# Performance work log

Hardware: AMD Instinct MI355X
Metric: run time of the kernel (lower is better)

## Reference

```python
import jax, jax.numpy as jnp
import numpy as np

# dims
C = 16      # input_channels
H = 64      # hidden_channels
HID = 128   # CDEFunc hidden width (hardcoded in source)
OUT = 1     # output_channels
L = 128     # number of time knots -> L-1 spline segments
B = 2048    # batch


def setup_inputs() -> dict:
    key = jax.random.key(0)
    ks = jax.random.split(key, 9)
    n = lambda k, shape, s: (jax.random.normal(k, shape, dtype=jnp.float32) * s)
    return {
        # cubic Hermite spline coeffs: concat(a, b, two_c, three_d) along last dim
        "coeffs": n(ks[0], (B, L - 1, 4 * C), 0.1),
        "W_init": n(ks[1], (H, C), 0.2),
        "b_init": jnp.zeros((H,), jnp.float32),
        "W1": n(ks[2], (HID, H), 0.1),
        "b1": jnp.zeros((HID,), jnp.float32),
        "W2": n(ks[3], (H * C, HID), 0.05),
        "b2": jnp.zeros((H * C,), jnp.float32),
        "W_out": n(ks[4], (OUT, H), 0.1),
        "b_out": jnp.zeros((OUT,), jnp.float32),
    }


def _spline_deriv(coeffs, t):
    """dX/dt of cubic spline at scalar time t. coeffs: (B, L-1, 4C)."""
    idx = jnp.clip(jnp.floor(t).astype(jnp.int32), 0, L - 2)
    seg = jax.lax.dynamic_slice_in_dim(coeffs, idx, 1, axis=1)[:, 0]  # (B, 4C)
    a, b, two_c, three_d = jnp.split(seg, 4, axis=-1)
    fr = t - idx.astype(t.dtype) if hasattr(t, 'dtype') else t - idx
    return b + two_c * fr + three_d * (fr * fr)  # (B, C)


def reference(coeffs, W_init, b_init, W1, b1, W2, b2, W_out, b_out):
    # X(0) = a of first segment (frac = 0)
    X0 = coeffs[:, 0, :C]
    z0 = X0 @ W_init.T + b_init  # (B, H)

    def f(z, dX):
        # CDEFunc: linear-relu-linear-tanh -> (B, H, C), then contract with dX/dt
        h = jax.nn.relu(z @ W1.T + b1)
        g = jnp.tanh(h @ W2.T + b2).reshape(-1, H, C)
        return jnp.einsum('bhc,bc->bh', g, dX)

    dt = jnp.float32(1.0)  # one RK4 step per knot interval

    def step(z, t):
        d0 = _spline_deriv(coeffs, t)
        dm = _spline_deriv(coeffs, t + 0.5 * dt)
        d1 = _spline_deriv(coeffs, t + dt)
        k1 = f(z, d0)
        k2 = f(z + 0.5 * dt * k1, dm)
        k3 = f(z + 0.5 * dt * k2, dm)
        k4 = f(z + dt * k3, d1)
        return z + (dt / 6.0) * (k1 + 2.0 * k2 + 2.0 * k3 + k4), None

    ts = jnp.arange(L - 1, dtype=jnp.float32)
    zT, _ = jax.lax.scan(step, z0, ts)
    return zT @ W_out.T + b_out  # (B, OUT)
```

## Files before the change

kernel.cpp:

```cpp
#include <hip/hip_runtime.h>

#define L_DIM 128
#define BB 8

typedef _Float16 f16;
typedef _Float16 f16x8 __attribute__((ext_vector_type(8)));
typedef float f32x4 __attribute__((ext_vector_type(4)));

__device__ __forceinline__ float fast_tanh_b(float x, float bk) {
    float e = __builtin_amdgcn_exp2f(fmaf(x, 2.8853900817779268f, bk));
    float r = __builtin_amdgcn_rcpf(e + 1.0f);
    return fmaf(-2.0f, r, 1.0f);
}

__attribute__((amdgpu_flat_work_group_size(512, 512), amdgpu_waves_per_eu(2)))
__global__ void
cde_kernel(const float* __restrict__ coeffs,
           const float* __restrict__ W_init, const float* __restrict__ b_init,
           const float* __restrict__ W1, const float* __restrict__ b1,
           const float* __restrict__ W2, const float* __restrict__ b2,
           const float* __restrict__ W_out, const float* __restrict__ b_out,
           float* __restrict__ out)
{
    __shared__ __align__(16) f16   z16[16][72];
    __shared__ __align__(16) f16   h16[16][136];
    __shared__ __align__(16) float dxT[2][3][16][20];
    __shared__ __align__(16) float zf[BB][64];

    const int tid  = threadIdx.x;
    const int blk  = blockIdx.x;
    const int lane = tid & 63;
    const int w    = tid >> 6;
    const int q    = lane >> 4;
    const int lr   = lane & 15;
    const int hh   = w * 8 + (lr & 7);
    const int chp  = lr >> 3;
    const int row0 = (q & 1) * 4 + (q >> 1) * 2;

    f16x8 w2f[8][4];
    float b2k[8];
#pragma unroll
    for (int t8 = 0; t8 < 8; ++t8) {
        const int outc = hh * 16 + 2 * t8 + chp;
        b2k[t8] = 2.8853900817779268f * b2[outc];
#pragma unroll
        for (int kc = 0; kc < 4; ++kc) {
            const float* src = W2 + (size_t)outc * 128 + kc * 32 + q * 8;
            f16x8 v;
#pragma unroll
            for (int i = 0; i < 8; ++i) v[i] = (f16)src[i];
            w2f[t8][kc] = v;
        }
    }
    f16x8 w1f[2];
#pragma unroll
    for (int kc = 0; kc < 2; ++kc) {
        const float* src = W1 + (size_t)(w * 16 + lr) * 64 + kc * 32 + q * 8;
        f16x8 v;
#pragma unroll
        for (int i = 0; i < 8; ++i) v[i] = (f16)src[i];
        w1f[kc] = v;
    }
    const float b1r = b1[w * 16 + lr];

    float z32r[2], ksumr[2];
#pragma unroll
    for (int j = 0; j < 2; ++j) {
        const float* x0 = coeffs + (size_t)(blk * BB + row0 + j) * (L_DIM - 1) * 64;
        float a = b_init[hh];
#pragma unroll
        for (int c = 0; c < 16; ++c) a = fmaf(x0[c], W_init[hh * 16 + c], a);
        z32r[j] = a;
        ksumr[j] = 0.f;
        if (lr < 8) z16[row0 + j][hh] = (f16)a;
    }
    for (int i = tid; i < 8 * 72; i += 512) z16[8 + i / 72][i % 72] = (f16)0.f;
    if (tid < BB * 16) {
        const int b = tid >> 4, c = tid & 15;
        const float* seg = coeffs + (size_t)(blk * BB + b) * (L_DIM - 1) * 64;
        float bv = seg[16 + c], cv = seg[32 + c], dv = seg[48 + c];
        dxT[0][0][c][b] = bv;
        dxT[0][1][c][b] = fmaf(0.25f, dv, fmaf(0.5f, cv, bv));
        dxT[0][2][c][b] = seg[64 + 16 + c];
    }
    __syncthreads();

    for (int t = 0; t < L_DIM - 1; ++t) {
        const int buf = t & 1;
        float pb = 0.f, pc = 0.f, pd = 0.f, pe = 0.f;
#pragma unroll 1
        for (int s = 0; s < 4; ++s) {
            {
                f16x8 za0 = *(const f16x8*)&z16[lr][q * 8];
                f16x8 za1 = *(const f16x8*)&z16[lr][32 + q * 8];
                f32x4 hacc = {0.f, 0.f, 0.f, 0.f};
                hacc = __builtin_amdgcn_mfma_f32_16x16x32_f16(za0, w1f[0], hacc, 0, 0, 0);
                hacc = __builtin_amdgcn_mfma_f32_16x16x32_f16(za1, w1f[1], hacc, 0, 0, 0);
#pragma unroll
                for (int r = 0; r < 4; ++r)
                    h16[q * 4 + r][w * 16 + lr] = (f16)fmaxf(hacc[r] + b1r, 0.f);
            }
            __syncthreads();

            const int ds = (s + 1) >> 1;
            const f16x8 af0 = *(const f16x8*)&h16[lr][q * 8];
            const f16x8 af1 = *(const f16x8*)&h16[lr][32 + q * 8];
            const f16x8 af2 = *(const f16x8*)&h16[lr][64 + q * 8];
            const f16x8 af3 = *(const f16x8*)&h16[lr][96 + q * 8];
            f32x4 acc[8];
#pragma unroll
            for (int t8 = 0; t8 < 8; ++t8) acc[t8] = (f32x4){0.f, 0.f, 0.f, 0.f};
#pragma unroll
            for (int tt = 0; tt < 4; ++tt) {
                acc[tt] = __builtin_amdgcn_mfma_f32_16x16x32_f16(af0, w2f[tt][0], acc[tt], 0, 0, 0);
                acc[tt] = __builtin_amdgcn_mfma_f32_16x16x32_f16(af1, w2f[tt][1], acc[tt], 0, 0, 0);
                acc[tt] = __builtin_amdgcn_mfma_f32_16x16x32_f16(af2, w2f[tt][2], acc[tt], 0, 0, 0);
                acc[tt] = __builtin_amdgcn_mfma_f32_16x16x32_f16(af3, w2f[tt][3], acc[tt], 0, 0, 0);
            }
#pragma unroll
            for (int tt = 4; tt < 8; ++tt) {
                acc[tt] = __builtin_amdgcn_mfma_f32_16x16x32_f16(af0, w2f[tt][0], acc[tt], 0, 0, 0);
                acc[tt] = __builtin_amdgcn_mfma_f32_16x16x32_f16(af1, w2f[tt][1], acc[tt], 0, 0, 0);
                acc[tt] = __builtin_amdgcn_mfma_f32_16x16x32_f16(af2, w2f[tt][2], acc[tt], 0, 0, 0);
                acc[tt] = __builtin_amdgcn_mfma_f32_16x16x32_f16(af3, w2f[tt][3], acc[tt], 0, 0, 0);
            }
            if (s == 2 && t < L_DIM - 2 && tid < 128) {
                const int b = tid >> 4, c = tid & 15;
                const float* seg = coeffs + ((size_t)(blk * BB + b) * (L_DIM - 1) + (t + 1)) * 64;
                pb = seg[16 + c]; pc = seg[32 + c]; pd = seg[48 + c];
                pe = (t + 1 < L_DIM - 2) ? seg[80 + c] : 0.f;
            }
            float2 dvv[8];
#pragma unroll
            for (int t8 = 0; t8 < 8; ++t8)
                dvv[t8] = *(const float2*)&dxT[buf][ds][2 * t8 + chp][row0];
            float ka0 = 0.f, ka1 = 0.f;
#pragma unroll
            for (int t8 = 0; t8 < 8; ++t8) {
                float u0 = __shfl_xor(acc[t8][2], 32);
                float u1 = __shfl_xor(acc[t8][3], 32);
                float g0 = fast_tanh_b((lane < 32) ? acc[t8][0] : u0, b2k[t8]);
                float g1 = fast_tanh_b((lane < 32) ? acc[t8][1] : u1, b2k[t8]);
                ka0 = fmaf(g0, dvv[t8].x, ka0);
                ka1 = fmaf(g1, dvv[t8].y, ka1);
            }
            ka0 += __shfl_xor(ka0, 8);
            ka1 += __shfl_xor(ka1, 8);
            float zs0, zs1;
            if (s == 3) {
                z32r[0] = fmaf(ksumr[0] + ka0, 1.f / 6.f, z32r[0]); zs0 = z32r[0];
                z32r[1] = fmaf(ksumr[1] + ka1, 1.f / 6.f, z32r[1]); zs1 = z32r[1];
            } else {
                ksumr[0] = (s == 0) ? ka0 : fmaf(2.f, ka0, ksumr[0]);
                ksumr[1] = (s == 0) ? ka1 : fmaf(2.f, ka1, ksumr[1]);
                const float alpha = (s == 2) ? 1.f : 0.5f;
                zs0 = fmaf(alpha, ka0, z32r[0]);
                zs1 = fmaf(alpha, ka1, z32r[1]);
            }
            if (lr < 8) {
                z16[row0 + 0][hh] = (f16)zs0;
                z16[row0 + 1][hh] = (f16)zs1;
            }
            if (s == 3 && t < L_DIM - 2 && tid < 128) {
                const int b = tid >> 4, c = tid & 15;
                dxT[buf ^ 1][0][c][b] = pb;
                dxT[buf ^ 1][1][c][b] = fmaf(0.25f, pd, fmaf(0.5f, pc, pb));
                dxT[buf ^ 1][2][c][b] = (t + 1 < L_DIM - 2) ? pe : (pb + pc + pd);
            }
            __syncthreads();
        }
    }

    if (lr < 8) {
        zf[row0 + 0][hh] = z32r[0];
        zf[row0 + 1][hh] = z32r[1];
    }
    __syncthreads();
    if (tid < 64) {
        const int b = lane >> 3, j0 = lane & 7;
        float p = 0.f;
#pragma unroll
        for (int m = 0; m < 8; ++m) p += zf[b][j0 + 8 * m] * W_out[j0 + 8 * m];
        p += __shfl_xor(p, 1, 64);
        p += __shfl_xor(p, 2, 64);
        p += __shfl_xor(p, 4, 64);
        if (j0 == 0) out[blk * BB + b] = p + b_out[0];
    }
}

extern "C" void kernel_launch(void* const* d_in, const int* in_sizes, int n_in,
                              void* d_out, int out_size, void* d_ws, size_t ws_size,
                              hipStream_t stream) {
    const float* coeffs = (const float*)d_in[0];
    const float* W_init = (const float*)d_in[1];
    const float* b_init = (const float*)d_in[2];
    const float* W1     = (const float*)d_in[3];
    const float* b1     = (const float*)d_in[4];
    const float* W2     = (const float*)d_in[5];
    const float* b2     = (const float*)d_in[6];
    const float* W_out  = (const float*)d_in[7];
    const float* b_out  = (const float*)d_in[8];
    cde_kernel<<<256, 512, 0, stream>>>(coeffs, W_init, b_init, W1, b1, W2, b2,
                                        W_out, b_out, (float*)d_out);
}
```

Before: 789.3 us.

## Double block to 1024 threads, halving per-wave W2 columns and offloading prefetch

Each block now runs 16 waves, and each wave owns 4 hidden units instead of 8. That halves the W2 register fragments and the MFMA chain per wave, so more waves can hide latency within the same batch tile. Only the first 8 waves compute the first-layer GEMM, while the upper waves prefetch the next spline segment and write the dX buffers. The inner RK stage loop is now fully unrolled. In exchange there are twice as many threads at each barrier, the W1 stage leaves half the waves idle, and the reduction needs an extra shuffle.

After: 928.5 us. 1.18x slower.

```diff
diff --git a/kernel.cpp b/kernel.cpp
--- a/kernel.cpp
+++ b/kernel.cpp
@@ -13,7 +13,7 @@
     return fmaf(-2.0f, r, 1.0f);
 }
 
-__attribute__((amdgpu_flat_work_group_size(512, 512), amdgpu_waves_per_eu(2)))
+__attribute__((amdgpu_flat_work_group_size(1024, 1024), amdgpu_waves_per_eu(4)))
 __global__ void
 cde_kernel(const float* __restrict__ coeffs,
            const float* __restrict__ W_init, const float* __restrict__ b_init,
@@ -33,35 +33,38 @@
     const int w    = tid >> 6;
     const int q    = lane >> 4;
     const int lr   = lane & 15;
-    const int hh   = w * 8 + (lr & 7);
-    const int chp  = lr >> 3;
+    const int hh   = 4 * w + (lr & 3);
+    const int cq   = lr >> 2;
     const int row0 = (q & 1) * 4 + (q >> 1) * 2;
 
-    f16x8 w2f[8][4];
-    float b2k[8];
+    f16x8 w2f[4][4];
+    float b2k[4];
 #pragma unroll
-    for (int t8 = 0; t8 < 8; ++t8) {
-        const int outc = hh * 16 + 2 * t8 + chp;
-        b2k[t8] = 2.8853900817779268f * b2[outc];
+    for (int tau = 0; tau < 4; ++tau) {
+        const int outc = hh * 16 + 4 * tau + cq;
+        b2k[tau] = 2.8853900817779268f * b2[outc];
 #pragma unroll
         for (int kc = 0; kc < 4; ++kc) {
             const float* src = W2 + (size_t)outc * 128 + kc * 32 + q * 8;
             f16x8 v;
 #pragma unroll
             for (int i = 0; i < 8; ++i) v[i] = (f16)src[i];
-            w2f[t8][kc] = v;
+            w2f[tau][kc] = v;
         }
     }
     f16x8 w1f[2];
+    float b1r = 0.f;
+    if (w < 8) {
 #pragma unroll
-    for (int kc = 0; kc < 2; ++kc) {
-        const float* src = W1 + (size_t)(w * 16 + lr) * 64 + kc * 32 + q * 8;
-        f16x8 v;
+        for (int kc = 0; kc < 2; ++kc) {
+            const float* src = W1 + (size_t)(w * 16 + lr) * 64 + kc * 32 + q * 8;
+            f16x8 v;
 #pragma unroll
-        for (int i = 0; i < 8; ++i) v[i] = (f16)src[i];
-        w1f[kc] = v;
+            for (int i = 0; i < 8; ++i) v[i] = (f16)src[i];
+            w1f[kc] = v;
+        }
+        b1r = b1[w * 16 + lr];
     }
-    const float b1r = b1[w * 16 + lr];
 
     float z32r[2], ksumr[2];
 #pragma unroll
@@ -72,9 +75,9 @@
         for (int c = 0; c < 16; ++c) a = fmaf(x0[c], W_init[hh * 16 + c], a);
         z32r[j] = a;
         ksumr[j] = 0.f;
-        if (lr < 8) z16[row0 + j][hh] = (f16)a;
+        if (lr < 4) z16[row0 + j][hh] = (f16)a;
     }
-    for (int i = tid; i < 8 * 72; i += 512) z16[8 + i / 72][i % 72] = (f16)0.f;
+    for (int i = tid; i < 8 * 72; i += 1024) z16[8 + i / 72][i % 72] = (f16)0.f;
     if (tid < BB * 16) {
         const int b = tid >> 4, c = tid & 15;
         const float* seg = coeffs + (size_t)(blk * BB + b) * (L_DIM - 1) * 64;
@@ -88,9 +91,9 @@
     for (int t = 0; t < L_DIM - 1; ++t) {
         const int buf = t & 1;
         float pb = 0.f, pc = 0.f, pd = 0.f, pe = 0.f;
-#pragma unroll 1
+#pragma unroll
         for (int s = 0; s < 4; ++s) {
-            {
+            if (w < 8) {
                 f16x8 za0 = *(const f16x8*)&z16[lr][q * 8];
                 f16x8 za1 = *(const f16x8*)&z16[lr][32 + q * 8];
                 f32x4 hacc = {0.f, 0.f, 0.f, 0.f};
@@ -99,53 +102,41 @@
 #pragma unroll
                 for (int r = 0; r < 4; ++r)
                     h16[q * 4 + r][w * 16 + lr] = (f16)fmaxf(hacc[r] + b1r, 0.f);
+            } else if (s == 2 && t < L_DIM - 2) {
+                const int pt = tid - 512;
+                if (pt < BB * 16) {
+                    const int b = pt >> 4, c = pt & 15;
+                    const float* seg = coeffs + ((size_t)(blk * BB + b) * (L_DIM - 1) + (t + 1)) * 64;
+                    pb = seg[16 + c]; pc = seg[32 + c]; pd = seg[48 + c];
+                    pe = (t + 1 < L_DIM - 2) ? seg[80 + c] : 0.f;
+                }
             }
             __syncthreads();
 
             const int ds = (s + 1) >> 1;
-            const f16x8 af0 = *(const f16x8*)&h16[lr][q * 8];
-            const f16x8 af1 = *(const f16x8*)&h16[lr][32 + q * 8];
-            const f16x8 af2 = *(const f16x8*)&h16[lr][64 + q * 8];
-            const f16x8 af3 = *(const f16x8*)&h16[lr][96 + q * 8];
-            f32x4 acc[8];
+            f32x4 acc[4];
 #pragma unroll
-            for (int t8 = 0; t8 < 8; ++t8) acc[t8] = (f32x4){0.f, 0.f, 0.f, 0.f};
+            for (int tau = 0; tau < 4; ++tau) acc[tau] = (f32x4){0.f, 0.f, 0.f, 0.f};
 #pragma unroll
-            for (int tt = 0; tt < 4; ++tt) {
-                acc[tt] = __builtin_amdgcn_mfma_f32_16x16x32_f16(af0, w2f[tt][0], acc[tt], 0, 0, 0);
-                acc[tt] = __builtin_amdgcn_mfma_f32_16x16x32_f16(af1, w2f[tt][1], acc[tt], 0, 0, 0);
-                acc[tt] = __builtin_amdgcn_mfma_f32_16x16x32_f16(af2, w2f[tt][2], acc[tt], 0, 0, 0);
-                acc[tt] = __builtin_amdgcn_mfma_f32_16x16x32_f16(af3, w2f[tt][3], acc[tt], 0, 0, 0);
+            for (int kc = 0; kc < 4; ++kc) {
+                const f16x8 af = *(const f16x8*)&h16[lr][kc * 32 + q * 8];
+#pragma unroll
+                for (int tau = 0; tau < 4; ++tau)
+                    acc[tau] = __builtin_amdgcn_mfma_f32_16x16x32_f16(af, w2f[tau][kc], acc[tau], 0, 0, 0);
             }
-#pragma unroll
-            for (int tt = 4; tt < 8; ++tt) {
-                acc[tt] = __builtin_amdgcn_mfma_f32_16x16x32_f16(af0, w2f[tt][0], acc[tt], 0, 0, 0);
-                acc[tt] = __builtin_amdgcn_mfma_f32_16x16x32_f16(af1, w2f[tt][1], acc[tt], 0, 0, 0);
-                acc[tt] = __builtin_amdgcn_mfma_f32_16x16x32_f16(af2, w2f[tt][2], acc[tt], 0, 0, 0);
-                acc[tt] = __builtin_amdgcn_mfma_f32_16x16x32_f16(af3, w2f[tt][3], acc[tt], 0, 0, 0);
-            }
-            if (s == 2 && t < L_DIM - 2 && tid < 128) {
-                const int b = tid >> 4, c = tid & 15;
-                const float* seg = coeffs + ((size_t)(blk * BB + b) * (L_DIM - 1) + (t + 1)) * 64;
-                pb = seg[16 + c]; pc = seg[32 + c]; pd = seg[48 + c];
-                pe = (t + 1 < L_DIM - 2) ? seg[80 + c] : 0.f;
-            }
-            float2 dvv[8];
-#pragma unroll
-            for (int t8 = 0; t8 < 8; ++t8)
-                dvv[t8] = *(const float2*)&dxT[buf][ds][2 * t8 + chp][row0];
             float ka0 = 0.f, ka1 = 0.f;
 #pragma unroll
-            for (int t8 = 0; t8 < 8; ++t8) {
-                float u0 = __shfl_xor(acc[t8][2], 32);
-                float u1 = __shfl_xor(acc[t8][3], 32);
-                float g0 = fast_tanh_b((lane < 32) ? acc[t8][0] : u0, b2k[t8]);
-                float g1 = fast_tanh_b((lane < 32) ? acc[t8][1] : u1, b2k[t8]);
-                ka0 = fmaf(g0, dvv[t8].x, ka0);
-                ka1 = fmaf(g1, dvv[t8].y, ka1);
+            for (int tau = 0; tau < 4; ++tau) {
+                const float2 dvv = *(const float2*)&dxT[buf][ds][4 * tau + cq][row0];
+                float u0 = __shfl_xor(acc[tau][2], 32);
+                float u1 = __shfl_xor(acc[tau][3], 32);
+                float g0 = fast_tanh_b((lane < 32) ? acc[tau][0] : u0, b2k[tau]);
+                float g1 = fast_tanh_b((lane < 32) ? acc[tau][1] : u1, b2k[tau]);
+                ka0 = fmaf(g0, dvv.x, ka0);
+                ka1 = fmaf(g1, dvv.y, ka1);
             }
-            ka0 += __shfl_xor(ka0, 8);
-            ka1 += __shfl_xor(ka1, 8);
+            ka0 += __shfl_xor(ka0, 4);  ka0 += __shfl_xor(ka0, 8);
+            ka1 += __shfl_xor(ka1, 4);  ka1 += __shfl_xor(ka1, 8);
             float zs0, zs1;
             if (s == 3) {
                 z32r[0] = fmaf(ksumr[0] + ka0, 1.f / 6.f, z32r[0]); zs0 = z32r[0];
@@ -157,21 +148,24 @@
                 zs0 = fmaf(alpha, ka0, z32r[0]);
                 zs1 = fmaf(alpha, ka1, z32r[1]);
             }
-            if (lr < 8) {
+            if (lr < 4) {
                 z16[row0 + 0][hh] = (f16)zs0;
                 z16[row0 + 1][hh] = (f16)zs1;
             }
-            if (s == 3 && t < L_DIM - 2 && tid < 128) {
-                const int b = tid >> 4, c = tid & 15;
-                dxT[buf ^ 1][0][c][b] = pb;
-                dxT[buf ^ 1][1][c][b] = fmaf(0.25f, pd, fmaf(0.5f, pc, pb));
-                dxT[buf ^ 1][2][c][b] = (t + 1 < L_DIM - 2) ? pe : (pb + pc + pd);
+            if (s == 3 && t < L_DIM - 2 && w >= 8) {
+                const int pt = tid - 512;
+                if (pt < BB * 16) {
+                    const int b = pt >> 4, c = pt & 15;
+                    dxT[buf ^ 1][0][c][b] = pb;
+                    dxT[buf ^ 1][1][c][b] = fmaf(0.25f, pd, fmaf(0.5f, pc, pb));
+                    dxT[buf ^ 1][2][c][b] = (t + 1 < L_DIM - 2) ? pe : (pb + pc + pd);
+                }
             }
             __syncthreads();
         }
     }
 
-    if (lr < 8) {
+    if (lr < 4) {
         zf[row0 + 0][hh] = z32r[0];
         zf[row0 + 1][hh] = z32r[1];
     }
@@ -200,6 +194,6 @@
     const float* b2     = (const float*)d_in[6];
     const float* W_out  = (const float*)d_in[7];
     const float* b_out  = (const float*)d_in[8];
-    cde_kernel<<<256, 512, 0, stream>>>(coeffs, W_init, b_init, W1, b1, W2, b2,
-                                        W_out, b_out, (float*)d_out);
+    cde_kernel<<<256, 1024, 0, stream>>>(coeffs, W_init, b_init, W1, b1, W2, b2,
+                                         W_out, b_out, (float*)d_out);
 }
```

## Split W2 MFMA into two halves interleaved with tanh, unroll RK4 stages

Applied to the files above, without the earlier changes.

Fully unrolls the four RK4 stage loop. Splits the second GEMM into two halves of four output tiles each, so the tanh/contraction epilogue of one half can overlap the MFMAs of the other. Odd waves raise their scheduling priority during the MFMA burst to stagger waves. The coeff prefetch moves to stage 1. Unrolling raises code size and register pressure, and the priority tweak may change how waves interleave.

After: 755.4 us. 1.04x faster.

```diff
diff --git a/kernel.cpp b/kernel.cpp
--- a/kernel.cpp
+++ b/kernel.cpp
@@ -88,7 +88,7 @@
     for (int t = 0; t < L_DIM - 1; ++t) {
         const int buf = t & 1;
         float pb = 0.f, pc = 0.f, pd = 0.f, pe = 0.f;
-#pragma unroll 1
+#pragma unroll
         for (int s = 0; s < 4; ++s) {
             {
                 f16x8 za0 = *(const f16x8*)&z16[lr][q * 8];
@@ -103,46 +103,41 @@
             __syncthreads();
 
             const int ds = (s + 1) >> 1;
-            const f16x8 af0 = *(const f16x8*)&h16[lr][q * 8];
-            const f16x8 af1 = *(const f16x8*)&h16[lr][32 + q * 8];
-            const f16x8 af2 = *(const f16x8*)&h16[lr][64 + q * 8];
-            const f16x8 af3 = *(const f16x8*)&h16[lr][96 + q * 8];
-            f32x4 acc[8];
-#pragma unroll
-            for (int t8 = 0; t8 < 8; ++t8) acc[t8] = (f32x4){0.f, 0.f, 0.f, 0.f};
-#pragma unroll
-            for (int tt = 0; tt < 4; ++tt) {
-                acc[tt] = __builtin_amdgcn_mfma_f32_16x16x32_f16(af0, w2f[tt][0], acc[tt], 0, 0, 0);
-                acc[tt] = __builtin_amdgcn_mfma_f32_16x16x32_f16(af1, w2f[tt][1], acc[tt], 0, 0, 0);
-                acc[tt] = __builtin_amdgcn_mfma_f32_16x16x32_f16(af2, w2f[tt][2], acc[tt], 0, 0, 0);
-                acc[tt] = __builtin_amdgcn_mfma_f32_16x16x32_f16(af3, w2f[tt][3], acc[tt], 0, 0, 0);
-            }
-#pragma unroll
-            for (int tt = 4; tt < 8; ++tt) {
-                acc[tt] = __builtin_amdgcn_mfma_f32_16x16x32_f16(af0, w2f[tt][0], acc[tt], 0, 0, 0);
-                acc[tt] = __builtin_amdgcn_mfma_f32_16x16x32_f16(af1, w2f[tt][1], acc[tt], 0, 0, 0);
-                acc[tt] = __builtin_amdgcn_mfma_f32_16x16x32_f16(af2, w2f[tt][2], acc[tt], 0, 0, 0);
-                acc[tt] = __builtin_amdgcn_mfma_f32_16x16x32_f16(af3, w2f[tt][3], acc[tt], 0, 0, 0);
-            }
-            if (s == 2 && t < L_DIM - 2 && tid < 128) {
-                const int b = tid >> 4, c = tid & 15;
-                const float* seg = coeffs + ((size_t)(blk * BB + b) * (L_DIM - 1) + (t + 1)) * 64;
-                pb = seg[16 + c]; pc = seg[32 + c]; pd = seg[48 + c];
-                pe = (t + 1 < L_DIM - 2) ? seg[80 + c] : 0.f;
-            }
-            float2 dvv[8];
-#pragma unroll
-            for (int t8 = 0; t8 < 8; ++t8)
-                dvv[t8] = *(const float2*)&dxT[buf][ds][2 * t8 + chp][row0];
             float ka0 = 0.f, ka1 = 0.f;
 #pragma unroll
-            for (int t8 = 0; t8 < 8; ++t8) {
-                float u0 = __shfl_xor(acc[t8][2], 32);
-                float u1 = __shfl_xor(acc[t8][3], 32);
-                float g0 = fast_tanh_b((lane < 32) ? acc[t8][0] : u0, b2k[t8]);
-                float g1 = fast_tanh_b((lane < 32) ? acc[t8][1] : u1, b2k[t8]);
-                ka0 = fmaf(g0, dvv[t8].x, ka0);
-                ka1 = fmaf(g1, dvv[t8].y, ka1);
+            for (int hf = 0; hf < 2; ++hf) {
+                float2 dvv[4];
+#pragma unroll
+                for (int tt = 0; tt < 4; ++tt)
+                    dvv[tt] = *(const float2*)&dxT[buf][ds][2 * (hf * 4 + tt) + chp][row0];
+                f32x4 acc[4];
+#pragma unroll
+                for (int tt = 0; tt < 4; ++tt)
+                    acc[tt] = (f32x4){0.f, 0.f, 0.f, 0.f};
+                if (w & 1) __builtin_amdgcn_s_setprio(1);
+#pragma unroll
+                for (int kc = 0; kc < 4; ++kc) {
+                    f16x8 af = *(const f16x8*)&h16[lr][kc * 32 + q * 8];
+#pragma unroll
+                    for (int tt = 0; tt < 4; ++tt)
+                        acc[tt] = __builtin_amdgcn_mfma_f32_16x16x32_f16(af, w2f[hf * 4 + tt][kc], acc[tt], 0, 0, 0);
+                }
+                if (w & 1) __builtin_amdgcn_s_setprio(0);
+                if (hf == 0 && s == 1 && t < L_DIM - 2 && tid < 128) {
+                    const int b = tid >> 4, c = tid & 15;
+                    const float* seg = coeffs + ((size_t)(blk * BB + b) * (L_DIM - 1) + (t + 1)) * 64;
+                    pb = seg[16 + c]; pc = seg[32 + c]; pd = seg[48 + c];
+                    pe = (t + 1 < L_DIM - 2) ? seg[80 + c] : 0.f;
+                }
+#pragma unroll
+                for (int tt = 0; tt < 4; ++tt) {
+                    float u0 = __shfl_xor(acc[tt][2], 32);
+                    float u1 = __shfl_xor(acc[tt][3], 32);
+                    float g0 = fast_tanh_b((lane < 32) ? acc[tt][0] : u0, b2k[hf * 4 + tt]);
+                    float g1 = fast_tanh_b((lane < 32) ? acc[tt][1] : u1, b2k[hf * 4 + tt]);
+                    ka0 = fmaf(g0, dvv[tt].x, ka0);
+                    ka1 = fmaf(g1, dvv[tt].y, ka1);
+                }
             }
             ka0 += __shfl_xor(ka0, 8);
             ka1 += __shfl_xor(ka1, 8);
```
